# Kernel optimization log

Measured on AMD Instinct MI355X. Metric: run time of the kernel, lower is better.

Reference implementation:

```python
import jax, jax.numpy as jnp
import numpy as np

T, B, H, E, V, L = 256, 32, 1024, 1024, 32000, 2


def lstm_stack(x, h0, c0, Wih, Whh, bih, bhh):
    # x: [T,B,E]; Wih/Whh: [L,4H,H]; bih/bhh: [L,4H]; h0/c0: [L,B,H]
    for l in range(Wih.shape[0]):
        Wi, Wh, bi, bh = Wih[l], Whh[l], bih[l], bhh[l]

        def step(carry, xt, Wi=Wi, Wh=Wh, bi=bi, bh=bh):
            h, c = carry
            g = xt @ Wi.T + h @ Wh.T + bi + bh  # [B,4H]
            i_, f_, g_, o_ = jnp.split(g, 4, axis=-1)  # PyTorch gate order i,f,g,o
            c = jax.nn.sigmoid(f_) * c + jax.nn.sigmoid(i_) * jnp.tanh(g_)
            h = jax.nn.sigmoid(o_) * jnp.tanh(c)
            return (h, c), h

        (_, _), x = jax.lax.scan(step, (h0[l], c0[l]), x)
    return x  # [T,B,H]


def setup_inputs() -> dict:
    key = jax.random.key(0)
    ks = jax.random.split(key, 20)
    u = lambda k, s: jax.random.uniform(k, s, jnp.float32, -0.1, 0.1)
    n = lambda k, s: 0.02 * jax.random.normal(k, s, jnp.float32)
    return {
        'data_left': jax.random.randint(ks[0], (T, B), 0, V),
        'data_right': jax.random.randint(ks[1], (T, B), 0, V),
        'h0_left': jnp.zeros((L, B, H), jnp.float32),
        'c0_left': jnp.zeros((L, B, H), jnp.float32),
        'h0_right': jnp.zeros((L, B, H), jnp.float32),
        'c0_right': jnp.zeros((L, B, H), jnp.float32),
        'emb': u(ks[2], (V, E)),
        'Wih_l': n(ks[3], (L, 4 * H, H)), 'Whh_l': n(ks[4], (L, 4 * H, H)),
        'bih_l': n(ks[5], (L, 4 * H)), 'bhh_l': n(ks[6], (L, 4 * H)),
        'Wih_r': n(ks[7], (L, 4 * H, H)), 'Whh_r': n(ks[8], (L, 4 * H, H)),
        'bih_r': n(ks[9], (L, 4 * H)), 'bhh_r': n(ks[10], (L, 4 * H)),
        'attn_w': n(ks[11], (1, 3 * H)), 'attn_b': n(ks[12], (1,)),
        'trans_w': n(ks[13], (H, 3 * H)), 'trans_b': n(ks[14], (H,)),
        'dec_w': u(ks[15], (V, H)), 'dec_b': jnp.zeros((V,), jnp.float32),
    }


def reference(data_left, data_right, h0_left, c0_left, h0_right, c0_right,
              emb, Wih_l, Whh_l, bih_l, bhh_l, Wih_r, Whh_r, bih_r, bhh_r,
              attn_w, attn_b, trans_w, trans_b, dec_w, dec_b):
    # Encode (dropout=0 -> identity). Right branch runs on the flipped sequence.
    xL = emb[data_left]                    # [T,B,E]
    xR = emb[data_right[::-1]]             # [T,B,E]
    outL = lstm_stack(xL, h0_left, c0_left, Wih_l, Whh_l, bih_l, bhh_l)   # [T,B,H]
    outR = lstm_stack(xR, h0_right, c0_right, Wih_r, Whh_r, bih_r, bhh_r)[::-1]

    # attn Linear(3H,1) splits into per-chunk projections: [left_i, right_i, ctx_k]
    w1, w2, w3 = jnp.split(attn_w[0], 3)   # each [H]
    a = outL @ w1 + outR @ w2 + attn_b[0]  # [T,B] query-dependent part
    sL = outL @ w3                          # [T,B]
    sR = outR @ w3                          # [T,B]

    # context for query i has fixed length T+1: k<=i -> outL[k], k>i -> outR[k-1]
    kk = jnp.arange(T + 1)
    ii = jnp.arange(T)
    maskL = kk[None, :] <= ii[:, None]      # [T,T+1]
    sL_pad = jnp.concatenate([sL, jnp.zeros((1, B), sL.dtype)], 0)   # [T+1,B]
    sR_sh = jnp.concatenate([jnp.zeros((1, B), sR.dtype), sR], 0)    # sR[k-1]
    ctx_s = jnp.where(maskL[:, :, None], sL_pad[None], sR_sh[None])  # [T,T+1,B]
    scores = jnp.tanh(a[:, None, :] + ctx_s)                          # [T,T+1,B]
    p = jax.nn.softmax(scores, axis=1)

    pL = p * maskL[:, :, None]
    pR = p * (~maskL)[:, :, None]
    # context_vector[i] = sum_k p[i,k] * ctx[i,k]
    cv = (jnp.einsum('ikb,kbh->ibh', pL[:, :T], outL)
          + jnp.einsum('ikb,kbh->ibh', pR[:, 1:], outR))              # [T,B,H]

    h3 = jnp.concatenate([outL, outR, cv], axis=-1)                   # [T,B,3H]
    pred = jnp.tanh(h3 @ trans_w.T + trans_b)                         # [T,B,H]
    decoded = pred @ dec_w.T + dec_b                                  # [T,B,V]
    return decoded
```

## Files before the change

kernel.cpp:

```cpp
#include <hip/hip_runtime.h>
#include <hip/hip_bf16.h>


using bf16 = __hip_bfloat16;
typedef __attribute__((ext_vector_type(8))) __bf16 bf16x8;
typedef __attribute__((ext_vector_type(4))) float f32x4;
typedef __attribute__((ext_vector_type(4))) short short4v;

#define T_ 256
#define B_ 32
#define H_ 1024
#define V_ 32000

__device__ __forceinline__ float b2f(bf16 x) { return __bfloat162float(x); }
__device__ __forceinline__ bf16 f2b(float x) { return __float2bfloat16(x); }
__device__ __forceinline__ float us2f(unsigned short u) {
  union { unsigned u; float f; } w; w.u = ((unsigned)u) << 16; return w.f;
}
__device__ __forceinline__ void st4(bf16* dst, float4 f) {
  union { bf16 h[4]; short4v s; } u;
  u.h[0] = f2b(f.x); u.h[1] = f2b(f.y); u.h[2] = f2b(f.z); u.h[3] = f2b(f.w);
  *reinterpret_cast<short4v*>(dst) = u.s;
}
__device__ __forceinline__ bf16x8 cvt8(float4 a, float4 b) {
  union { bf16 h[8]; bf16x8 v; } u;
  u.h[0] = f2b(a.x); u.h[1] = f2b(a.y); u.h[2] = f2b(a.z); u.h[3] = f2b(a.w);
  u.h[4] = f2b(b.x); u.h[5] = f2b(b.y); u.h[6] = f2b(b.z); u.h[7] = f2b(b.w);
  return u.v;
}
__device__ __forceinline__ void gload_lds16(const bf16* g, bf16* l) {
  __builtin_amdgcn_global_load_lds(
      (const __attribute__((address_space(1))) void*)g,
      (__attribute__((address_space(3))) void*)l, 16, 0, 0);
}

__global__ __launch_bounds__(256)
void cvt_f32_bf16(const float* __restrict__ src, bf16* __restrict__ dst, long n)
{
  long i = ((long)blockIdx.x * 256 + threadIdx.x) * 8;
  if (i >= n) return;
  float4 a = *reinterpret_cast<const float4*>(src + i);
  float4 b = *reinterpret_cast<const float4*>(src + i + 4);
  st4(dst + i, a); st4(dst + i + 4, b);
}

__global__ __launch_bounds__(128)
void embed_gather(const int* __restrict__ dl, const int* __restrict__ dr,
                  const float* __restrict__ emb,
                  bf16* __restrict__ xL, bf16* __restrict__ xR)
{
  int wg = blockIdx.x;
  int d  = wg >> 13;
  int r  = wg & 8191;
  int t  = r >> 5, b = r & 31;
  int tok = d ? dr[(T_ - 1 - t) * B_ + b] : dl[r];
  const float* src = emb + (long)tok * H_;
  bf16* dst = (d ? xR : xL) + (long)r * H_;
  int e = threadIdx.x * 8;
  float4 a = *reinterpret_cast<const float4*>(src + e);
  float4 c = *reinterpret_cast<const float4*>(src + e + 4);
  st4(dst + e, a); st4(dst + e + 4, c);
}

#define LSTRIDE 40

template<int ACT, int HASBIAS, int OUTF32>
__global__ __launch_bounds__(256)
void gemm_bt(const bf16* __restrict__ A, const float* __restrict__ Bwf,
             const float* __restrict__ bias, void* __restrict__ Cv,
             int M, int N, int K)
{
  __shared__ __align__(16) bf16 As[128 * LSTRIDE];
  __shared__ __align__(16) bf16 Bs[128 * LSTRIDE];
  const int tid  = threadIdx.x;
  const int lane = tid & 63;
  const int wave = tid >> 6;
  const int wm = wave >> 1, wn = wave & 1;
  const long bm = blockIdx.x, bn = blockIdx.y;

  const bf16*  Ag = A + bm * 128 * (long)K;
  const float* Bg = Bwf + bn * 128 * (long)K;

  f32x4 acc[4][4] = {};

  const int nk = K >> 5;
  for (int kt = 0; kt < nk; ++kt) {
    const int k0 = kt * 32;
    __syncthreads();
    #pragma unroll
    for (int j = 0; j < 2; ++j) {
      int chunk = j * 256 + tid;
      int row = chunk >> 2, c4 = chunk & 3;
      *reinterpret_cast<bf16x8*>(&As[row * LSTRIDE + c4 * 8]) =
          *reinterpret_cast<const bf16x8*>(&Ag[(long)row * K + k0 + c4 * 8]);
    }
    #pragma unroll
    for (int j = 0; j < 4; ++j) {
      int chunk = j * 256 + tid;
      int row = chunk >> 3, c4f = chunk & 7;
      float4 f = *reinterpret_cast<const float4*>(&Bg[(long)row * K + k0 + c4f * 4]);
      st4(&Bs[row * LSTRIDE + c4f * 4], f);
    }
    __syncthreads();
    bf16x8 af[4], bfr[4];
    #pragma unroll
    for (int m = 0; m < 4; ++m)
      af[m] = *reinterpret_cast<const bf16x8*>(
          &As[(wm * 64 + m * 16 + (lane & 15)) * LSTRIDE + (lane >> 4) * 8]);
    #pragma unroll
    for (int n = 0; n < 4; ++n)
      bfr[n] = *reinterpret_cast<const bf16x8*>(
          &Bs[(wn * 64 + n * 16 + (lane & 15)) * LSTRIDE + (lane >> 4) * 8]);
    #pragma unroll
    for (int m = 0; m < 4; ++m)
      #pragma unroll
      for (int n = 0; n < 4; ++n)
        acc[m][n] = __builtin_amdgcn_mfma_f32_16x16x32_bf16(af[m], bfr[n], acc[m][n], 0, 0, 0);
  }

  #pragma unroll
  for (int m = 0; m < 4; ++m) {
    int row = (int)bm * 128 + wm * 64 + m * 16 + ((lane >> 4) << 2);
    #pragma unroll
    for (int n = 0; n < 4; ++n) {
      int col = (int)bn * 128 + wn * 64 + n * 16 + (lane & 15);
      float bv = HASBIAS ? bias[col] : 0.f;
      #pragma unroll
      for (int j = 0; j < 4; ++j) {
        float v = acc[m][n][j] + bv;
        if (ACT) v = tanhf(v);
        long off = (long)(row + j) * N + col;
        if (OUTF32) reinterpret_cast<float*>(Cv)[off] = v;
        else        reinterpret_cast<bf16*>(Cv)[off] = f2b(v);
      }
    }
  }
}

template<int ACT, int HASBIAS, int OUTF32>
__global__ __launch_bounds__(512, 1)
void gemm8(const bf16* __restrict__ A, const bf16* __restrict__ Bw,
           const float* __restrict__ bias, void* __restrict__ Cv,
           int M, int N, int K, int mt)
{
  __shared__ __align__(16) bf16 As[2][256 * 64];
  __shared__ __align__(16) bf16 Bs[2][256 * 64];
  const int tid  = threadIdx.x;
  const int lane = tid & 63;
  const int wave = tid >> 6;
  const int wm = wave >> 2, wn = wave & 3;

  const int nwg = (int)gridDim.x;
  const int cpx = nwg >> 3;
  const int bid = (int)blockIdx.x;
  const int swz = (bid & 7) * cpx + (bid >> 3);
  const long bm = swz % mt, bn = swz / mt;

  const bf16* Ag = A  + bm * 256 * (long)K;
  const bf16* Bg = Bw + bn * 256 * (long)K;

  f32x4 acc[8][4] = {};
  const int nt = K >> 6;

  auto stage = [&](int buf, int kt) {
    const int k0 = kt * 64;
    #pragma unroll
    for (int g = 0; g < 8; ++g) {
      const int gl = g & 3;
      const int c  = gl * 512 + tid;
      const int r  = c >> 3;
      const int sl = (c & 7) ^ (r & 7);
      if (g < 4)
        gload_lds16(Ag + (long)r * K + k0 + sl * 8, &As[buf][gl * 4096 + wave * 512]);
      else
        gload_lds16(Bg + (long)r * K + k0 + sl * 8, &Bs[buf][gl * 4096 + wave * 512]);
    }
  };

  stage(0, 0);
  asm volatile("s_waitcnt vmcnt(0)" ::: "memory");
  __builtin_amdgcn_s_barrier();

  for (int j = 0; j < nt; ++j) {
    const int cur = j & 1, nxt = cur ^ 1;
    if (j + 1 < nt) {
      stage(nxt, j + 1);
      asm volatile("s_waitcnt vmcnt(8)" ::: "memory");
    } else {
      asm volatile("s_waitcnt vmcnt(0)" ::: "memory");
    }
    __builtin_amdgcn_s_barrier();

    bf16x8 bfr[4][2];
    #pragma unroll
    for (int fn = 0; fn < 4; ++fn)
      #pragma unroll
      for (int kk = 0; kk < 2; ++kk) {
        int rb = wn * 64 + fn * 16 + (lane & 15);
        int u  = (lane >> 4) + 4 * kk;
        bfr[fn][kk] = *reinterpret_cast<const bf16x8*>(
            &Bs[cur][rb * 64 + (u ^ (rb & 7)) * 8]);
      }

    #pragma unroll
    for (int p = 0; p < 4; ++p) {
      bf16x8 afr[2][2];
      #pragma unroll
      for (int q = 0; q < 2; ++q)
        #pragma unroll
        for (int kk = 0; kk < 2; ++kk) {
          int ra = wm * 128 + (p * 2 + q) * 16 + (lane & 15);
          int u  = (lane >> 4) + 4 * kk;
          afr[q][kk] = *reinterpret_cast<const bf16x8*>(
              &As[cur][ra * 64 + (u ^ (ra & 7)) * 8]);
        }
      __builtin_amdgcn_s_barrier();
      __builtin_amdgcn_s_setprio(1);
      #pragma unroll
      for (int q = 0; q < 2; ++q)
        #pragma unroll
        for (int fn = 0; fn < 4; ++fn) {
          acc[p * 2 + q][fn] = __builtin_amdgcn_mfma_f32_16x16x32_bf16(
              afr[q][0], bfr[fn][0], acc[p * 2 + q][fn], 0, 0, 0);
          acc[p * 2 + q][fn] = __builtin_amdgcn_mfma_f32_16x16x32_bf16(
              afr[q][1], bfr[fn][1], acc[p * 2 + q][fn], 0, 0, 0);
        }
      __builtin_amdgcn_s_setprio(0);
      __builtin_amdgcn_s_barrier();
    }
  }

  #pragma unroll
  for (int fm = 0; fm < 8; ++fm) {
    int row = (int)bm * 256 + wm * 128 + fm * 16 + ((lane >> 4) << 2);
    #pragma unroll
    for (int fn = 0; fn < 4; ++fn) {
      int col = (int)bn * 256 + wn * 64 + fn * 16 + (lane & 15);
      float bv = HASBIAS ? bias[col] : 0.f;
      #pragma unroll
      for (int jj = 0; jj < 4; ++jj) {
        float v = acc[fm][fn][jj] + bv;
        if (ACT) v = tanhf(v);
        long off = (long)(row + jj) * N + col;
        if (OUTF32) reinterpret_cast<float*>(Cv)[off] = v;
        else        reinterpret_cast<bf16*>(Cv)[off] = f2b(v);
      }
    }
  }
}

__global__ __launch_bounds__(256, 1)
void lstm_layer(const bf16* __restrict__ WhhL, const bf16* __restrict__ WhhR,
                const bf16* __restrict__ giL,  const bf16* __restrict__ giR,
                const float* __restrict__ bihL, const float* __restrict__ bhhL,
                const float* __restrict__ bihR, const float* __restrict__ bhhR,
                const float* __restrict__ h0L, const float* __restrict__ h0R,
                const float* __restrict__ c0L, const float* __restrict__ c0R,
                bf16* __restrict__ houtL, bf16* __restrict__ houtR,
                int revR, unsigned* __restrict__ bar)
{
  const int d    = blockIdx.y;
  const int u0   = blockIdx.x * 16;
  const int tid  = threadIdx.x;
  const int lane = tid & 63;
  const int wq   = tid >> 6;
  const long BH  = (long)B_ * H_;

  const bf16*  Whh = d ? WhhR : WhhL;
  const bf16*  gi0 = d ? giR  : giL;
  const float* bi  = d ? bihR : bihL;
  const float* bh  = d ? bhhR : bhhL;
  const float* h0  = d ? h0R  : h0L;
  const float* c0  = d ? c0R  : c0L;
  bf16* hout       = d ? houtR : houtL;
  const int rev    = d ? revR : 0;
  unsigned* cnt    = bar + d;

  (void)__hip_atomic_load(cnt, __ATOMIC_ACQUIRE, __HIP_MEMORY_SCOPE_AGENT);

  const int klo = (lane >> 4) * 8;

  bf16x8 w_reg[4][8];
  #pragma unroll
  for (int g = 0; g < 4; ++g) {
    const bf16* p = Whh + ((long)g * H_ + u0 + (lane & 15)) * H_ + wq * 256 + klo;
    #pragma unroll
    for (int q = 0; q < 8; ++q)
      w_reg[g][q] = *reinterpret_cast<const bf16x8*>(p + q * 32);
  }

  const int b  = tid >> 3;
  const int u  = (tid & 7) * 2;
  const int ug = u0 + u;

  float bsum[4][2];
  #pragma unroll
  for (int g = 0; g < 4; ++g) {
    bsum[g][0] = bi[g * H_ + ug]     + bh[g * H_ + ug];
    bsum[g][1] = bi[g * H_ + ug + 1] + bh[g * H_ + ug + 1];
  }
  float cc0 = c0[(long)b * H_ + ug];
  float cc1 = c0[(long)b * H_ + ug + 1];

  __shared__ float gbuf[4][4][32][16];

  for (int s = 0; s < T_; ++s) {
    unsigned giv[4];
    {
      const bf16* gis = gi0 + (long)s * (B_ * 4 * H_) + (long)b * (4 * H_);
      #pragma unroll
      for (int g = 0; g < 4; ++g)
        giv[g] = *reinterpret_cast<const unsigned*>(&gis[g * H_ + ug]);
    }

    f32x4 acc[4][2];
    #pragma unroll
    for (int g = 0; g < 4; ++g) {
      acc[g][0] = f32x4{0.f, 0.f, 0.f, 0.f};
      acc[g][1] = f32x4{0.f, 0.f, 0.f, 0.f};
    }

    if (s == 0) {
      const float* ap0 = h0 + (long)(lane & 15) * H_ + wq * 256 + klo;
      const float* ap1 = ap0 + 16L * H_;
      #pragma unroll
      for (int q = 0; q < 8; ++q) {
        bf16x8 a0 = cvt8(*reinterpret_cast<const float4*>(ap0 + q * 32),
                         *reinterpret_cast<const float4*>(ap0 + q * 32 + 4));
        bf16x8 a1 = cvt8(*reinterpret_cast<const float4*>(ap1 + q * 32),
                         *reinterpret_cast<const float4*>(ap1 + q * 32 + 4));
        #pragma unroll
        for (int g = 0; g < 4; ++g) {
          acc[g][0] = __builtin_amdgcn_mfma_f32_16x16x32_bf16(a0, w_reg[g][q], acc[g][0], 0, 0, 0);
          acc[g][1] = __builtin_amdgcn_mfma_f32_16x16x32_bf16(a1, w_reg[g][q], acc[g][1], 0, 0, 0);
        }
      }
    } else {
      const bf16* hp  = hout + (long)(rev ? (T_ - s) : (s - 1)) * BH;
      const bf16* ap0 = hp + (long)(lane & 15) * H_ + wq * 256 + klo;
      const bf16* ap1 = ap0 + 16L * H_;
      #pragma unroll
      for (int q = 0; q < 8; ++q) {
        bf16x8 a0 = *reinterpret_cast<const bf16x8*>(ap0 + q * 32);
        bf16x8 a1 = *reinterpret_cast<const bf16x8*>(ap1 + q * 32);
        #pragma unroll
        for (int g = 0; g < 4; ++g) {
          acc[g][0] = __builtin_amdgcn_mfma_f32_16x16x32_bf16(a0, w_reg[g][q], acc[g][0], 0, 0, 0);
          acc[g][1] = __builtin_amdgcn_mfma_f32_16x16x32_bf16(a1, w_reg[g][q], acc[g][1], 0, 0, 0);
        }
      }
    }

    {
      int cr = (lane >> 4) << 2, ccu = lane & 15;
      #pragma unroll
      for (int g = 0; g < 4; ++g)
        #pragma unroll
        for (int j = 0; j < 4; ++j) {
          gbuf[wq][g][cr + j][ccu]      = acc[g][0][j];
          gbuf[wq][g][16 + cr + j][ccu] = acc[g][1][j];
        }
    }
    __syncthreads();

    {
      float g4[4][2];
      #pragma unroll
      for (int g = 0; g < 4; ++g) {
        float p0 = gbuf[0][g][b][u]     + gbuf[1][g][b][u];
        float p1 = gbuf[2][g][b][u]     + gbuf[3][g][b][u];
        float q0 = gbuf[0][g][b][u + 1] + gbuf[1][g][b][u + 1];
        float q1 = gbuf[2][g][b][u + 1] + gbuf[3][g][b][u + 1];
        g4[g][0] = (p0 + p1) + us2f((unsigned short)(giv[g] & 0xffffu)) + bsum[g][0];
        g4[g][1] = (q0 + q1) + us2f((unsigned short)(giv[g] >> 16))     + bsum[g][1];
      }
      float si0 = 1.f / (1.f + expf(-g4[0][0])), si1 = 1.f / (1.f + expf(-g4[0][1]));
      float sf0 = 1.f / (1.f + expf(-g4[1][0])), sf1 = 1.f / (1.f + expf(-g4[1][1]));
      float tg0 = tanhf(g4[2][0]),               tg1 = tanhf(g4[2][1]);
      float so0 = 1.f / (1.f + expf(-g4[3][0])), so1 = 1.f / (1.f + expf(-g4[3][1]));
      cc0 = sf0 * cc0 + si0 * tg0;
      cc1 = sf1 * cc1 + si1 * tg1;
      float hn0 = so0 * tanhf(cc0);
      float hn1 = so1 * tanhf(cc1);
      union { bf16 h[2]; unsigned w; } up;
      up.h[0] = f2b(hn0); up.h[1] = f2b(hn1);
      long wIdx = rev ? (long)(T_ - 1 - s) : (long)s;
      __hip_atomic_store(
          reinterpret_cast<unsigned*>(&hout[wIdx * BH + (long)b * H_ + ug]),
          up.w, __ATOMIC_RELAXED, __HIP_MEMORY_SCOPE_AGENT);
    }

    if (s + 1 < T_) {
      __syncthreads();
      if (tid == 0) {
        __hip_atomic_fetch_add(cnt, 1u, __ATOMIC_RELAXED, __HIP_MEMORY_SCOPE_AGENT);
        unsigned tgt = 64u * (unsigned)(s + 1);
        while (__hip_atomic_load(cnt, __ATOMIC_RELAXED, __HIP_MEMORY_SCOPE_AGENT) < tgt)
          __builtin_amdgcn_s_sleep(2);
      }
      __syncthreads();
    }
  }
}

__global__ __launch_bounds__(256)
void attn_scores(const bf16* __restrict__ outL, const bf16* __restrict__ outR,
                 const float* __restrict__ attn_w, const float* __restrict__ attn_b,
                 float* __restrict__ a, float* __restrict__ sL, float* __restrict__ sR)
{
  int r = blockIdx.x;
  int tid = threadIdx.x;
  const bf16* oL = outL + (long)r * H_;
  const bf16* oR = outR + (long)r * H_;
  int e = tid * 4;
  float pa = 0.f, pl = 0.f, pr = 0.f;
  #pragma unroll
  for (int j = 0; j < 4; ++j) {
    float l_ = b2f(oL[e + j]), r_ = b2f(oR[e + j]);
    float w1 = attn_w[e + j];
    float w2 = attn_w[H_ + e + j];
    float w3 = attn_w[2 * H_ + e + j];
    pa += w1 * l_ + w2 * r_;
    pl += w3 * l_;
    pr += w3 * r_;
  }
  #pragma unroll
  for (int off = 32; off > 0; off >>= 1) {
    pa += __shfl_down(pa, off);
    pl += __shfl_down(pl, off);
    pr += __shfl_down(pr, off);
  }
  __shared__ float red[3][4];
  int wave = tid >> 6, lane = tid & 63;
  if (lane == 0) { red[0][wave] = pa; red[1][wave] = pl; red[2][wave] = pr; }
  __syncthreads();
  if (tid == 0) {
    a[r]  = red[0][0] + red[0][1] + red[0][2] + red[0][3] + attn_b[0];
    sL[r] = red[1][0] + red[1][1] + red[1][2] + red[1][3];
    sR[r] = red[2][0] + red[2][1] + red[2][2] + red[2][3];
  }
}

__global__ __launch_bounds__(64)
void attn_softmax(const float* __restrict__ a, const float* __restrict__ sL,
                  const float* __restrict__ sR, float* __restrict__ p)
{
  int i = blockIdx.x, b = blockIdx.y;
  int lane = threadIdx.x;
  float av = a[i * B_ + b];
  float sc[5];
  float mx = -1e30f;
  #pragma unroll
  for (int q = 0; q < 5; ++q) {
    int k = lane + q * 64;
    float v = -1e30f;
    if (k < 257) {
      float ctx = (k <= i) ? sL[k * B_ + b] : sR[(k - 1) * B_ + b];
      v = tanhf(av + ctx);
    }
    sc[q] = v;
    mx = fmaxf(mx, v);
  }
  #pragma unroll
  for (int off = 32; off > 0; off >>= 1) mx = fmaxf(mx, __shfl_xor(mx, off));
  float sum = 0.f;
  #pragma unroll
  for (int q = 0; q < 5; ++q) {
    int k = lane + q * 64;
    float e = (k < 257) ? __expf(sc[q] - mx) : 0.f;
    sc[q] = e; sum += e;
  }
  #pragma unroll
  for (int off = 32; off > 0; off >>= 1) sum += __shfl_xor(sum, off);
  float inv = 1.f / sum;
  long base = ((long)b * T_ + i) * 257;
  #pragma unroll
  for (int q = 0; q < 5; ++q) {
    int k = lane + q * 64;
    if (k < 257) p[base + k] = sc[q] * inv;
  }
}

__global__ __launch_bounds__(256)
void h3_copy(const bf16* __restrict__ outL, const bf16* __restrict__ outR,
             bf16* __restrict__ h3)
{
  long gid = (long)blockIdx.x * 256 + threadIdx.x;
  long e = gid * 8;
  if (e >= (long)T_ * B_ * H_) return;
  long r = e >> 10; int h = (int)(e & 1023);
  *reinterpret_cast<bf16x8*>(&h3[r * 3 * H_ + h]) =
      *reinterpret_cast<const bf16x8*>(&outL[e]);
  *reinterpret_cast<bf16x8*>(&h3[r * 3 * H_ + H_ + h]) =
      *reinterpret_cast<const bf16x8*>(&outR[e]);
}

__global__ __launch_bounds__(256)
void attn_cv(const float* __restrict__ p, const bf16* __restrict__ outL,
             const bf16* __restrict__ outR, bf16* __restrict__ h3)
{
  int b = blockIdx.y;
  int i0 = blockIdx.x * 16;
  int tid = threadIdx.x;
  __shared__ float ps[16][257];
  for (int idx = tid; idx < 16 * 257; idx += 256) {
    int ii = idx / 257, k = idx % 257;
    ps[ii][k] = p[((long)b * T_ + i0 + ii) * 257 + k];
  }
  __syncthreads();
  float acc[16][4] = {};
  int h0 = tid * 4;
  for (int k = 0; k < 257; ++k) {
    float vL[4] = {0.f, 0.f, 0.f, 0.f}, vR[4] = {0.f, 0.f, 0.f, 0.f};
    if (k < 256) {
      short4v v = *reinterpret_cast<const short4v*>(&outL[((long)k * B_ + b) * H_ + h0]);
      vL[0] = us2f((unsigned short)v[0]); vL[1] = us2f((unsigned short)v[1]);
      vL[2] = us2f((unsigned short)v[2]); vL[3] = us2f((unsigned short)v[3]);
    }
    if (k >= 1) {
      short4v v = *reinterpret_cast<const short4v*>(&outR[((long)(k - 1) * B_ + b) * H_ + h0]);
      vR[0] = us2f((unsigned short)v[0]); vR[1] = us2f((unsigned short)v[1]);
      vR[2] = us2f((unsigned short)v[2]); vR[3] = us2f((unsigned short)v[3]);
    }
    #pragma unroll
    for (int ii = 0; ii < 16; ++ii) {
      float pv = ps[ii][k];
      bool useL = (i0 + ii) >= k;
      #pragma unroll
      for (int j = 0; j < 4; ++j)
        acc[ii][j] += pv * (useL ? vL[j] : vR[j]);
    }
  }
  #pragma unroll
  for (int ii = 0; ii < 16; ++ii)
    #pragma unroll
    for (int j = 0; j < 4; ++j)
      h3[((long)(i0 + ii) * B_ + b) * 3 * H_ + 2 * H_ + h0 + j] = f2b(acc[ii][j]);
}

extern "C" void kernel_launch(void* const* d_in, const int* in_sizes, int n_in,
                              void* d_out, int out_size, void* d_ws, size_t ws_size,
                              hipStream_t stream)
{
  (void)in_sizes; (void)n_in; (void)out_size;
  const int*   data_left  = (const int*)  d_in[0];
  const int*   data_right = (const int*)  d_in[1];
  const float* h0_left    = (const float*)d_in[2];
  const float* c0_left    = (const float*)d_in[3];
  const float* h0_right   = (const float*)d_in[4];
  const float* c0_right   = (const float*)d_in[5];
  const float* emb        = (const float*)d_in[6];
  const float* Wih_l      = (const float*)d_in[7];
  const float* Whh_l      = (const float*)d_in[8];
  const float* bih_l      = (const float*)d_in[9];
  const float* bhh_l      = (const float*)d_in[10];
  const float* Wih_r      = (const float*)d_in[11];
  const float* Whh_r      = (const float*)d_in[12];
  const float* bih_r      = (const float*)d_in[13];
  const float* bhh_r      = (const float*)d_in[14];
  const float* attn_w     = (const float*)d_in[15];
  const float* attn_b     = (const float*)d_in[16];
  const float* trans_w    = (const float*)d_in[17];
  const float* trans_b    = (const float*)d_in[18];
  const float* dec_w      = (const float*)d_in[19];
  const float* dec_b      = (const float*)d_in[20];

  char* ws = (char*)d_ws;
  bf16*     XL   = (bf16*)    (ws + 0L);
  bf16*     XR   = (bf16*)    (ws + 16777216L);
  bf16*     GI_L = (bf16*)    (ws + 33554432L);
  bf16*     GI_R = (bf16*)    (ws + 100663296L);
  bf16*     H0L  = (bf16*)    (ws + 167772160L);
  bf16*     H0R  = (bf16*)    (ws + 184549376L);
  unsigned* BAR  = (unsigned*)(ws + 201326592L);
  bf16*     WHHB = (bf16*)    (ws + 201588736L);
  bf16*     WIHB   = (bf16*)  (ws + 235143168L);
  bf16*     TRANSB = (bf16*)  (ws + 268697600L);
  bf16*     DECB   = (bf16*)  (ws + 274989056L);
  const bool fast = ws_size >= 340525056UL;
  bf16*  O1L  = XL;
  bf16*  O1R  = XR;
  bf16*  H3   = GI_L;
  float* P_   = (float*)(ws + 100663296L);
  float* A_   = (float*)(ws + 109084672L);
  float* SL_  = (float*)(ws + 109117440L);
  float* SR_  = (float*)(ws + 109150208L);
  bf16*  PRED = (bf16*) (ws + 109182976L);

  const long BH  = (long)B_ * H_;
  const long WL  = 4L * H_ * H_;
  bf16* WHHB_l = WHHB;
  bf16* WHHB_r = WHHB + 2 * WL;
  bf16* WIHB_l = WIHB;
  bf16* WIHB_r = WIHB + 2 * WL;

  cvt_f32_bf16<<<4096, 256, 0, stream>>>(Whh_l, WHHB_l, 2 * WL);
  cvt_f32_bf16<<<4096, 256, 0, stream>>>(Whh_r, WHHB_r, 2 * WL);
  if (fast) {
    cvt_f32_bf16<<<4096, 256, 0, stream>>>(Wih_l, WIHB_l, 2 * WL);
    cvt_f32_bf16<<<4096, 256, 0, stream>>>(Wih_r, WIHB_r, 2 * WL);
    cvt_f32_bf16<<<1536, 256, 0, stream>>>(trans_w, TRANSB, (long)H_ * 3 * H_);
    cvt_f32_bf16<<<16000, 256, 0, stream>>>(dec_w, DECB, (long)V_ * H_);
  }

  embed_gather<<<16384, 128, 0, stream>>>(data_left, data_right, emb, XL, XR);

  if (fast) {
    gemm8<0,0,0><<<512, 512, 0, stream>>>(XL, WIHB_l, nullptr, GI_L, 8192, 4096, 1024, 32);
    gemm8<0,0,0><<<512, 512, 0, stream>>>(XR, WIHB_r, nullptr, GI_R, 8192, 4096, 1024, 32);
  } else {
    gemm_bt<0,0,0><<<dim3(64, 32), 256, 0, stream>>>(XL, Wih_l, nullptr, GI_L, 8192, 4096, 1024);
    gemm_bt<0,0,0><<<dim3(64, 32), 256, 0, stream>>>(XR, Wih_r, nullptr, GI_R, 8192, 4096, 1024);
  }

  hipMemsetAsync(BAR, 0, 256, stream);
  lstm_layer<<<dim3(64, 2), 256, 0, stream>>>(
      WHHB_l, WHHB_r, GI_L, GI_R,
      bih_l, bhh_l, bih_r, bhh_r,
      h0_left, h0_right, c0_left, c0_right,
      H0L, H0R, 0, BAR);

  if (fast) {
    gemm8<0,0,0><<<512, 512, 0, stream>>>(H0L, WIHB_l + WL, nullptr, GI_L, 8192, 4096, 1024, 32);
    gemm8<0,0,0><<<512, 512, 0, stream>>>(H0R, WIHB_r + WL, nullptr, GI_R, 8192, 4096, 1024, 32);
  } else {
    gemm_bt<0,0,0><<<dim3(64, 32), 256, 0, stream>>>(H0L, Wih_l + WL, nullptr, GI_L, 8192, 4096, 1024);
    gemm_bt<0,0,0><<<dim3(64, 32), 256, 0, stream>>>(H0R, Wih_r + WL, nullptr, GI_R, 8192, 4096, 1024);
  }

  hipMemsetAsync(BAR, 0, 256, stream);
  lstm_layer<<<dim3(64, 2), 256, 0, stream>>>(
      WHHB_l + WL, WHHB_r + WL, GI_L, GI_R,
      bih_l + 4 * H_, bhh_l + 4 * H_, bih_r + 4 * H_, bhh_r + 4 * H_,
      h0_left + BH, h0_right + BH, c0_left + BH, c0_right + BH,
      O1L, O1R, 1, BAR);

  attn_scores<<<8192, 256, 0, stream>>>(O1L, O1R, attn_w, attn_b, A_, SL_, SR_);
  attn_softmax<<<dim3(256, 32), 64, 0, stream>>>(A_, SL_, SR_, P_);
  h3_copy<<<4096, 256, 0, stream>>>(O1L, O1R, H3);
  attn_cv<<<dim3(16, 32), 256, 0, stream>>>(P_, O1L, O1R, H3);

  if (fast) {
    gemm8<1,1,0><<<128, 512, 0, stream>>>(H3, TRANSB, trans_b, PRED, 8192, 1024, 3072, 32);
    gemm8<0,1,1><<<4000, 512, 0, stream>>>(PRED, DECB, dec_b, d_out, 8192, 32000, 1024, 32);
  } else {
    gemm_bt<1,1,0><<<dim3(64, 8),   256, 0, stream>>>(H3,   trans_w, trans_b, PRED, 8192, 1024, 3072);
    gemm_bt<0,1,1><<<dim3(64, 250), 256, 0, stream>>>(PRED, dec_w,   dec_b,   d_out, 8192, 32000, 1024);
  }
}
```

Baseline: 4.589 ms.

## Add 128x128 bf16 GEMM for mid-size GEMMs and prefetch LSTM gate inputs

Adds a smaller 128x128-tile single-buffered bf16 MFMA GEMM (gemm_bb). It replaces the 256x256 gemm8 for the input-projection and trans GEMMs, which gives more workgroups on the 8192x4096 and 8192x1024 shapes. In the LSTM recurrent kernel, the next step's precomputed gate inputs are now loaded before the grid-barrier spin, hiding global load latency on the serial critical path. The barrier arrive is also split from the wait. The new GEMM has no double buffering, so it may lose efficiency compared with the larger tiles.

```diff
diff --git a/kernel.cpp b/kernel.cpp
--- a/kernel.cpp
+++ b/kernel.cpp
@@ -138,6 +138,74 @@
 }
 
 template<int ACT, int HASBIAS, int OUTF32>
+__global__ __launch_bounds__(256)
+void gemm_bb(const bf16* __restrict__ A, const bf16* __restrict__ Bw,
+             const float* __restrict__ bias, void* __restrict__ Cv,
+             int M, int N, int K)
+{
+  __shared__ __align__(16) bf16 As[128 * 32];
+  __shared__ __align__(16) bf16 Bs[128 * 32];
+  const int tid  = threadIdx.x;
+  const int lane = tid & 63;
+  const int wave = tid >> 6;
+  const int wm = wave >> 1, wn = wave & 1;
+  const long bm = blockIdx.x, bn = blockIdx.y;
+
+  const bf16* Ag = A  + bm * 128 * (long)K;
+  const bf16* Bg = Bw + bn * 128 * (long)K;
+
+  const int r0  = tid >> 2;
+  const int cgd = (tid & 3) ^ (r0 & 3);
+  const int rsw = ((lane >> 4) ^ (lane & 3)) * 8;
+
+  f32x4 acc[4][4] = {};
+  const int nk = K >> 5;
+  for (int kt = 0; kt < nk; ++kt) {
+    const int k0 = kt * 32;
+    __syncthreads();
+    #pragma unroll
+    for (int j = 0; j < 2; ++j) {
+      int row = j * 64 + r0;
+      gload_lds16(Ag + (long)row * K + k0 + cgd * 8, As + (j * 256 + wave * 64) * 8);
+      gload_lds16(Bg + (long)row * K + k0 + cgd * 8, Bs + (j * 256 + wave * 64) * 8);
+    }
+    __syncthreads();
+    bf16x8 af[4], bfr[4];
+    #pragma unroll
+    for (int m = 0; m < 4; ++m)
+      af[m] = *reinterpret_cast<const bf16x8*>(
+          &As[(wm * 64 + m * 16 + (lane & 15)) * 32 + rsw]);
+    #pragma unroll
+    for (int n = 0; n < 4; ++n)
+      bfr[n] = *reinterpret_cast<const bf16x8*>(
+          &Bs[(wn * 64 + n * 16 + (lane & 15)) * 32 + rsw]);
+    #pragma unroll
+    for (int m = 0; m < 4; ++m)
+      #pragma unroll
+      for (int n = 0; n < 4; ++n)
+        acc[m][n] = __builtin_amdgcn_mfma_f32_16x16x32_bf16(af[m], bfr[n], acc[m][n], 0, 0, 0);
+  }
+
+  #pragma unroll
+  for (int m = 0; m < 4; ++m) {
+    int row = (int)bm * 128 + wm * 64 + m * 16 + ((lane >> 4) << 2);
+    #pragma unroll
+    for (int n = 0; n < 4; ++n) {
+      int col = (int)bn * 128 + wn * 64 + n * 16 + (lane & 15);
+      float bv = HASBIAS ? bias[col] : 0.f;
+      #pragma unroll
+      for (int j = 0; j < 4; ++j) {
+        float v = acc[m][n][j] + bv;
+        if (ACT) v = tanhf(v);
+        long off = (long)(row + j) * N + col;
+        if (OUTF32) reinterpret_cast<float*>(Cv)[off] = v;
+        else        reinterpret_cast<bf16*>(Cv)[off] = f2b(v);
+      }
+    }
+  }
+}
+
+template<int ACT, int HASBIAS, int OUTF32>
 __global__ __launch_bounds__(512, 1)
 void gemm8(const bf16* __restrict__ A, const bf16* __restrict__ Bw,
            const float* __restrict__ bias, void* __restrict__ Cv,
@@ -265,6 +333,7 @@
   const int lane = tid & 63;
   const int wq   = tid >> 6;
   const long BH  = (long)B_ * H_;
+  const long B4H = (long)B_ * 4 * H_;
 
   const bf16*  Whh = d ? WhhR : WhhL;
   const bf16*  gi0 = d ? giR  : giL;
@@ -304,15 +373,15 @@
 
   __shared__ float gbuf[4][4][32][16];
 
+  unsigned giv[4];
+  {
+    const bf16* gis = gi0 + (long)b * (4 * H_);
+    #pragma unroll
+    for (int g = 0; g < 4; ++g)
+      giv[g] = *reinterpret_cast<const unsigned*>(&gis[g * H_ + ug]);
+  }
+
   for (int s = 0; s < T_; ++s) {
-    unsigned giv[4];
-    {
-      const bf16* gis = gi0 + (long)s * (B_ * 4 * H_) + (long)b * (4 * H_);
-      #pragma unroll
-      for (int g = 0; g < 4; ++g)
-        giv[g] = *reinterpret_cast<const unsigned*>(&gis[g * H_ + ug]);
-    }
-
     f32x4 acc[4][2];
     #pragma unroll
     for (int g = 0; g < 4; ++g) {
@@ -392,13 +461,23 @@
 
     if (s + 1 < T_) {
       __syncthreads();
+      if (tid == 0)
+        __hip_atomic_fetch_add(cnt, 1u, __ATOMIC_RELAXED, __HIP_MEMORY_SCOPE_AGENT);
+      unsigned ngiv[4];
+      {
+        const bf16* gis = gi0 + (long)(s + 1) * B4H + (long)b * (4 * H_);
+        #pragma unroll
+        for (int g = 0; g < 4; ++g)
+          ngiv[g] = *reinterpret_cast<const unsigned*>(&gis[g * H_ + ug]);
+      }
       if (tid == 0) {
-        __hip_atomic_fetch_add(cnt, 1u, __ATOMIC_RELAXED, __HIP_MEMORY_SCOPE_AGENT);
         unsigned tgt = 64u * (unsigned)(s + 1);
         while (__hip_atomic_load(cnt, __ATOMIC_RELAXED, __HIP_MEMORY_SCOPE_AGENT) < tgt)
           __builtin_amdgcn_s_sleep(2);
       }
       __syncthreads();
+      #pragma unroll
+      for (int g = 0; g < 4; ++g) giv[g] = ngiv[g];
     }
   }
 }
@@ -606,8 +685,8 @@
   embed_gather<<<16384, 128, 0, stream>>>(data_left, data_right, emb, XL, XR);
 
   if (fast) {
-    gemm8<0,0,0><<<512, 512, 0, stream>>>(XL, WIHB_l, nullptr, GI_L, 8192, 4096, 1024, 32);
-    gemm8<0,0,0><<<512, 512, 0, stream>>>(XR, WIHB_r, nullptr, GI_R, 8192, 4096, 1024, 32);
+    gemm_bb<0,0,0><<<dim3(64, 32), 256, 0, stream>>>(XL, WIHB_l, nullptr, GI_L, 8192, 4096, 1024);
+    gemm_bb<0,0,0><<<dim3(64, 32), 256, 0, stream>>>(XR, WIHB_r, nullptr, GI_R, 8192, 4096, 1024);
   } else {
     gemm_bt<0,0,0><<<dim3(64, 32), 256, 0, stream>>>(XL, Wih_l, nullptr, GI_L, 8192, 4096, 1024);
     gemm_bt<0,0,0><<<dim3(64, 32), 256, 0, stream>>>(XR, Wih_r, nullptr, GI_R, 8192, 4096, 1024);
@@ -621,8 +700,8 @@
       H0L, H0R, 0, BAR);
 
   if (fast) {
-    gemm8<0,0,0><<<512, 512, 0, stream>>>(H0L, WIHB_l + WL, nullptr, GI_L, 8192, 4096, 1024, 32);
-    gemm8<0,0,0><<<512, 512, 0, stream>>>(H0R, WIHB_r + WL, nullptr, GI_R, 8192, 4096, 1024, 32);
+    gemm_bb<0,0,0><<<dim3(64, 32), 256, 0, stream>>>(H0L, WIHB_l + WL, nullptr, GI_L, 8192, 4096, 1024);
+    gemm_bb<0,0,0><<<dim3(64, 32), 256, 0, stream>>>(H0R, WIHB_r + WL, nullptr, GI_R, 8192, 4096, 1024);
   } else {
     gemm_bt<0,0,0><<<dim3(64, 32), 256, 0, stream>>>(H0L, Wih_l + WL, nullptr, GI_L, 8192, 4096, 1024);
     gemm_bt<0,0,0><<<dim3(64, 32), 256, 0, stream>>>(H0R, Wih_r + WL, nullptr, GI_R, 8192, 4096, 1024);
@@ -641,7 +720,7 @@
   attn_cv<<<dim3(16, 32), 256, 0, stream>>>(P_, O1L, O1R, H3);
 
   if (fast) {
-    gemm8<1,1,0><<<128, 512, 0, stream>>>(H3, TRANSB, trans_b, PRED, 8192, 1024, 3072, 32);
+    gemm_bb<1,1,0><<<dim3(64, 8), 256, 0, stream>>>(H3, TRANSB, trans_b, PRED, 8192, 1024, 3072);
     gemm8<0,1,1><<<4000, 512, 0, stream>>>(PRED, DECB, dec_b, d_out, 8192, 32000, 1024, 32);
   } else {
     gemm_bt<1,1,0><<<dim3(64, 8),   256, 0, stream>>>(H3,   trans_w, trans_b, PRED, 8192, 1024, 3072);
```

Result: faster. 4.468 ms (-2.6%).
